# Performance work log

Measured on AMD Instinct MI355X. Metric: run time of the kernel, lower is better.

Reference implementation:

```python
import jax, jax.numpy as jnp
import numpy as np

N_NODES = 100000
N_EDGES = 1600000
IN_DIM = 64
OUT_DIM = 64
K_HEADS = 4
HEAD_DIM = OUT_DIM // K_HEADS


def setup_inputs() -> dict:
    key = jax.random.key(0)
    ks = jax.random.split(key, 12)
    x = jax.random.normal(ks[0], (N_NODES, IN_DIM), dtype=jnp.float32)
    edge_index = jax.random.randint(ks[1], (2, N_EDGES), 0, N_NODES, dtype=jnp.int64)
    edge_sign = jax.random.randint(ks[2], (N_EDGES,), 0, 2, dtype=jnp.int64)
    s = 1.0 / np.sqrt(IN_DIM)
    Wl_w = jax.random.uniform(ks[3], (OUT_DIM, IN_DIM), minval=-s, maxval=s, dtype=jnp.float32)
    Wl_b = jax.random.uniform(ks[4], (OUT_DIM,), minval=-s, maxval=s, dtype=jnp.float32)
    sign_tab = jax.random.normal(ks[5], (2, HEAD_DIM), dtype=jnp.float32)
    so = 1.0 / np.sqrt(OUT_DIM)
    Wh_w = jax.random.uniform(ks[6], (OUT_DIM, OUT_DIM), minval=-so, maxval=so, dtype=jnp.float32)
    Wh_b = jax.random.uniform(ks[7], (OUT_DIM,), minval=-so, maxval=so, dtype=jnp.float32)
    mlp_w1 = jax.random.uniform(ks[8], (OUT_DIM, OUT_DIM), minval=-so, maxval=so, dtype=jnp.float32)
    mlp_b1 = jax.random.uniform(ks[9], (OUT_DIM,), minval=-so, maxval=so, dtype=jnp.float32)
    mlp_w2 = jax.random.uniform(ks[10], (OUT_DIM, OUT_DIM), minval=-so, maxval=so, dtype=jnp.float32)
    mlp_b2 = jax.random.uniform(ks[11], (OUT_DIM,), minval=-so, maxval=so, dtype=jnp.float32)
    eps = jnp.zeros((1,), dtype=jnp.float32)
    return {"x": x, "edge_index": edge_index, "edge_sign": edge_sign,
            "Wl_w": Wl_w, "Wl_b": Wl_b, "sign_tab": sign_tab,
            "Wh_w": Wh_w, "Wh_b": Wh_b, "mlp_w1": mlp_w1, "mlp_b1": mlp_b1,
            "mlp_w2": mlp_w2, "mlp_b2": mlp_b2, "eps": eps}


def reference(x, edge_index, edge_sign, Wl_w, Wl_b, sign_tab, Wh_w, Wh_b,
              mlp_w1, mlp_b1, mlp_w2, mlp_b2, eps):
    N = x.shape[0]
    row, col = edge_index[0], edge_index[1]
    h = x @ Wl_w.T + Wl_b                              # [N, out_dim]
    hr = h.reshape(N, K_HEADS, HEAD_DIM)               # [N, K, hd]
    h_i = hr[row]                                      # [E, K, hd]
    h_j = hr[col]                                      # [E, K, hd]
    s_emb = sign_tab[edge_sign][:, None, :]            # [E, 1, hd]
    score = jnp.sum(h_i * h_j * s_emb, axis=-1)        # [E, K]
    # segment softmax over edges grouped by target node (row)
    mx = jax.ops.segment_max(score, row, num_segments=N)
    mx = jnp.where(jnp.isfinite(mx), mx, 0.0)          # empty segments -> 0
    ex = jnp.exp(score - mx[row])                      # [E, K]
    den = jax.ops.segment_sum(ex, row, num_segments=N)
    alpha = ex / (den[row] + 1e-16)                    # [E, K]
    # scatter-add weighted messages per head (vectorized over heads)
    msg = h_j * alpha[:, :, None]                      # [E, K, hd]
    aggr = jax.ops.segment_sum(msg, row, num_segments=N)  # [N, K, hd]
    m_l = aggr.reshape(N, OUT_DIM) @ Wh_w.T + Wh_b
    z = (1.0 + eps) * h + m_l
    hid = jax.nn.relu(z @ mlp_w1.T + mlp_b1)
    return hid @ mlp_w2.T + mlp_b2
```

## Files before the change

### kernel.cpp

```cpp
#include <hip/hip_runtime.h>

#define DIM 64
#define NBUCK 256
#define BSHIFT 9
#define BCAP 12288
#define CHUNK 4096

typedef __attribute__((ext_vector_type(4))) float f32x4;
typedef __attribute__((ext_vector_type(2))) float f32x2v;
typedef __attribute__((ext_vector_type(8))) short short8;

#define MFMA16(a, b, c) __builtin_amdgcn_mfma_f32_16x16x32_bf16(a, b, c, 0, 0, 0)

template <int CTRL>
__device__ __forceinline__ float qperm(float v) {
    return __int_as_float(__builtin_amdgcn_update_dpp(
        0, __float_as_int(v), CTRL, 0xF, 0xF, true));
}

__device__ __forceinline__ void cvt8(const float* f, short8& hi, short8& lo) {
#pragma unroll
    for (int e = 0; e < 8; ++e) {
        const unsigned u = __float_as_uint(f[e]);
        hi[e] = (short)(u >> 16);
        const float hf = __uint_as_float(u & 0xFFFF0000u);
        lo[e] = (short)(__float_as_uint(f[e] - hf) >> 16);
    }
}

__device__ __forceinline__ unsigned short bf16rne(float f) {
    const unsigned u = __float_as_uint(f);
    return (unsigned short)((u + 0x7FFFu + ((u >> 16) & 1u)) >> 16);
}

__global__ __launch_bounds__(256) void prep_kernel(
    const float* __restrict__ Wl, const float* __restrict__ Wh,
    const float* __restrict__ W1, const float* __restrict__ W2,
    short8* __restrict__ wf, int* __restrict__ bcursor,
    int* __restrict__ edata, int* __restrict__ offsets, int N, int E)
{
    const int tid = threadIdx.x;
    bcursor[tid] = 0;
    edata[E + tid] = 0;
    edata[E + 256 + tid] = 0;
    if (tid == 0) offsets[N] = E;
    const int m = tid >> 6, l = tid & 63;
    const float* W = (m == 0) ? Wl : (m == 1) ? Wh : (m == 2) ? W1 : W2;
    const int o = l & 15;
    const int kg = (l >> 4) * 8;
#pragma unroll
    for (int t = 0; t < 4; ++t)
#pragma unroll
        for (int s = 0; s < 2; ++s) {
            float f[8];
#pragma unroll
            for (int e = 0; e < 8; ++e)
                f[e] = W[(o + 16 * t) * DIM + 32 * s + kg + e];
            short8 hi, lo;
            cvt8(f, hi, lo);
            const int base = (((m * 4 + t) * 2 + s) * 2);
            wf[(base + 0) * 64 + l] = hi;
            wf[(base + 1) * 64 + l] = lo;
        }
}

__global__ __launch_bounds__(256, 3) void gemmbin_kernel(
    const float* __restrict__ x, const short8* __restrict__ wf,
    const float* __restrict__ bias, float* __restrict__ h,
    unsigned short* __restrict__ hb, int N,
    const int* __restrict__ ei, const int* __restrict__ sgn,
    int* __restrict__ bcursor, int* __restrict__ records, int E, int NB)
{
    if (blockIdx.x & 1) {
        const int l = threadIdx.x & 63;
        const int gw = (blockIdx.x >> 1) * 4 + (threadIdx.x >> 6);
        const int nw = NB * 4;
        const int nstrips = (N + 15) >> 4;
        const int lr = l & 15, lk = (l >> 4) * 8, lrow4 = (l >> 4) * 4;

        short8 wh_[4][2], wl_[4][2];
#pragma unroll
        for (int t = 0; t < 4; ++t)
#pragma unroll
            for (int s = 0; s < 2; ++s) {
                wh_[t][s] = wf[(((0 * 4 + t) * 2 + s) * 2 + 0) * 64 + l];
                wl_[t][s] = wf[(((0 * 4 + t) * 2 + s) * 2 + 1) * 64 + l];
            }
        float b4[4];
#pragma unroll
        for (int t = 0; t < 4; ++t) b4[t] = bias[lr + 16 * t];

        for (int strip = gw; strip < nstrips; strip += nw) {
            const int rbase = strip * 16;
            const int arow = min(rbase + lr, N - 1);
            short8 ah[2], al[2];
#pragma unroll
            for (int s = 0; s < 2; ++s) {
                const float4 p0 = *reinterpret_cast<const float4*>(x + (size_t)arow * DIM + 32 * s + lk);
                const float4 p1 = *reinterpret_cast<const float4*>(x + (size_t)arow * DIM + 32 * s + lk + 4);
                float f[8] = {p0.x, p0.y, p0.z, p0.w, p1.x, p1.y, p1.z, p1.w};
                cvt8(f, ah[s], al[s]);
            }
            f32x4 acc[4];
#pragma unroll
            for (int t = 0; t < 4; ++t) acc[t] = (f32x4){b4[t], b4[t], b4[t], b4[t]};
#pragma unroll
            for (int s = 0; s < 2; ++s) {
#pragma unroll
                for (int t = 0; t < 4; ++t) acc[t] = MFMA16(ah[s], wh_[t][s], acc[t]);
#pragma unroll
                for (int t = 0; t < 4; ++t) acc[t] = MFMA16(ah[s], wl_[t][s], acc[t]);
#pragma unroll
                for (int t = 0; t < 4; ++t) acc[t] = MFMA16(al[s], wh_[t][s], acc[t]);
            }
#pragma unroll
            for (int t = 0; t < 4; ++t)
#pragma unroll
                for (int rg = 0; rg < 4; ++rg) {
                    const int row = rbase + lrow4 + rg;
                    if (row < N) {
                        h[(size_t)row * DIM + lr + 16 * t] = acc[t][rg];
                        hb[(size_t)row * DIM + lr + 16 * t] = bf16rne(acc[t][rg]);
                    }
                }
        }
    } else {
        const int tid = threadIdx.x;
        const int base = (blockIdx.x >> 1) * CHUNK;
        __shared__ int lcnt[NBUCK];
        __shared__ int lbase[NBUCK];
        lcnt[tid] = 0;
        __syncthreads();
        const int lim = min(CHUNK, E - base);
        if (lim == CHUNK && (E & 3) == 0) {
            int r[16];
#pragma unroll
            for (int j = 0; j < 4; ++j) {
                const int4 a = *(reinterpret_cast<const int4*>(ei + base) + tid * 4 + j);
                r[4*j+0]=a.x; r[4*j+1]=a.y; r[4*j+2]=a.z; r[4*j+3]=a.w;
            }
#pragma unroll
            for (int i = 0; i < 16; ++i) atomicAdd(&lcnt[r[i] >> BSHIFT], 1);
            __syncthreads();
            const int c = lcnt[tid];
            lbase[tid] = c ? atomicAdd(&bcursor[tid], c) : 0;
            lcnt[tid] = 0;
            __syncthreads();
            int cc[16], ss[16];
#pragma unroll
            for (int j = 0; j < 4; ++j) {
                const int4 a = *(reinterpret_cast<const int4*>(ei + E + base) + tid * 4 + j);
                cc[4*j+0]=a.x; cc[4*j+1]=a.y; cc[4*j+2]=a.z; cc[4*j+3]=a.w;
                const int4 s2 = *(reinterpret_cast<const int4*>(sgn + base) + tid * 4 + j);
                ss[4*j+0]=s2.x; ss[4*j+1]=s2.y; ss[4*j+2]=s2.z; ss[4*j+3]=s2.w;
            }
#pragma unroll
            for (int half = 0; half < 2; ++half) {
                int idx[8];
#pragma unroll
                for (int i = 0; i < 8; ++i) {
                    const int e8 = half * 8 + i;
                    const int bkt = r[e8] >> BSHIFT;
                    idx[i] = lbase[bkt] + atomicAdd(&lcnt[bkt], 1);
                }
#pragma unroll
                for (int i = 0; i < 8; ++i) {
                    const int e8 = half * 8 + i;
                    const int bkt = r[e8] >> BSHIFT;
                    records[bkt * BCAP + min(idx[i], BCAP - 1)] =
                        cc[e8] | (ss[e8] << 17) | ((r[e8] & 511) << 18);
                }
            }
        } else {
            for (int k = tid; k < lim; k += 256)
                atomicAdd(&lcnt[ei[base + k] >> BSHIFT], 1);
            __syncthreads();
            const int c = lcnt[tid];
            lbase[tid] = c ? atomicAdd(&bcursor[tid], c) : 0;
            lcnt[tid] = 0;
            __syncthreads();
            for (int k = tid; k < lim; k += 256) {
                const int e = base + k;
                const int rr = ei[e];
                const int cc2 = ei[E + e];
                const int s = sgn[e];
                const int b = rr >> BSHIFT;
                const int idx = min(lbase[b] + atomicAdd(&lcnt[b], 1), BCAP - 1);
                records[b * BCAP + idx] = cc2 | (s << 17) | ((rr & 511) << 18);
            }
        }
    }
}

__device__ __forceinline__ int wave_incl_scan(int v, int lane) {
#pragma unroll
    for (int off = 1; off < 64; off <<= 1) {
        int t = __shfl_up(v, (unsigned)off, 64);
        if (lane >= off) v += t;
    }
    return v;
}

__global__ __launch_bounds__(256) void build_kernel(
    const int* __restrict__ records, const int* __restrict__ bcursor,
    int* __restrict__ offsets, int* __restrict__ edata, int N)
{
    const int b = blockIdx.x;
    const int tid = threadIdx.x, lane = tid & 63, w = tid >> 6;
    const int nbase = b << BSHIFT;
    const int nn = min(512, N - nbase);
    if (nn <= 0) return;

    __shared__ int ncnt[512];
    __shared__ int wtot[8];
    __shared__ int csrb_l[NBUCK];
    __shared__ int stag[BCAP];

    {
        const int bv = min(bcursor[tid], BCAP);
        const int inc = wave_incl_scan(bv, lane);
        if (lane == 63) wtot[w] = inc;
        __syncthreads();
        int add = 0;
#pragma unroll
        for (int i = 0; i < 4; ++i)
            if (i < w) add += wtot[i];
        csrb_l[tid] = add + inc - bv;
        __syncthreads();
    }
    const int base_csr = csrb_l[b];
    const int cnt = min(bcursor[b], BCAP);
    const int* rec = records + b * BCAP;

    ncnt[tid] = 0; ncnt[256 + tid] = 0;
    __syncthreads();
    for (int i = tid; i < cnt; i += 256)
        atomicAdd(&ncnt[rec[i] >> 18], 1);
    __syncthreads();
    const int v0 = ncnt[tid], v1 = ncnt[256 + tid];
    const int i0 = wave_incl_scan(v0, lane);
    if (lane == 63) wtot[w] = i0;
    const int i1 = wave_incl_scan(v1, lane);
    if (lane == 63) wtot[4 + w] = i1;
    __syncthreads();
    int a0 = 0, a1 = 0;
#pragma unroll
    for (int i = 0; i < 4; ++i) {
        if (i < w) { a0 += wtot[i]; a1 += wtot[4 + i]; }
    }
    const int half = wtot[0] + wtot[1] + wtot[2] + wtot[3];
    const int e0 = a0 + i0 - v0;
    const int e1 = half + a1 + i1 - v1;
    if (tid < nn)       offsets[nbase + tid]       = base_csr + e0;
    if (256 + tid < nn) offsets[nbase + 256 + tid] = base_csr + e1;
    __syncthreads();
    ncnt[tid] = e0; ncnt[256 + tid] = e1;
    __syncthreads();
    for (int i = tid; i < cnt; i += 256) {
        const int rcd = rec[i];
        const int p = atomicAdd(&ncnt[rcd >> 18], 1);
        stag[p] = (rcd & 0x1FFFF) | (((rcd >> 17) & 1) << 20);
    }
    __syncthreads();
    for (int i = tid; i < cnt; i += 256)
        edata[base_csr + i] = stag[i];
}

__global__ __launch_bounds__(256) void attntail_kernel(
    const float* __restrict__ h, const unsigned short* __restrict__ hb,
    const int* __restrict__ offsets, const int* __restrict__ edata,
    const float* __restrict__ sign_tab, const short8* __restrict__ wf,
    const float* __restrict__ bh, const float* __restrict__ b1,
    const float* __restrict__ b2, const float* __restrict__ eps,
    float* __restrict__ out, int N)
{
    __shared__ float bufA[16 * 68];
    __shared__ float bufB[16 * 68];

    const int lane = threadIdx.x & 63;
    const int w    = threadIdx.x >> 6;
    const int gl   = lane & 15;
    const int g    = lane >> 4;
    const int rbase = blockIdx.x * 16;
    const int node  = rbase + (w << 2) + g;
    const bool alive = node < N;
    const int nidx = alive ? node : 0;

    const int beg = offsets[nidx];
    const int deg = offsets[nidx + 1] - beg;

    const float4 hi = *reinterpret_cast<const float4*>(h + ((unsigned)nidx << 6) + (gl << 2));
    const float4 s0 = *reinterpret_cast<const float4*>(sign_tab + ((gl & 3) << 2));
    const float4 s1 = *reinterpret_cast<const float4*>(sign_tab + 16 + ((gl & 3) << 2));
    const f32x2v hs0a = {hi.x * s0.x, hi.y * s0.y};
    const f32x2v hs0b = {hi.z * s0.z, hi.w * s0.w};
    const f32x2v hs1a = {hi.x * s1.x, hi.y * s1.y};
    const f32x2v hs1b = {hi.z * s1.z, hi.w * s1.w};

    int maxdeg = max(deg, __shfl_xor(deg, 16, 64));
    maxdeg = max(maxdeg, __shfl_xor(maxdeg, 32, 64));

    float den = 0.f;
    f32x2v ma = {0.f, 0.f}, mb = {0.f, 0.f};
    const unsigned glb = (unsigned)(gl << 3);

    for (int e = 0; e < maxdeg; e += 8) {
        int pk[8];
#pragma unroll
        for (int u = 0; u < 8; ++u)
            pk[u] = edata[(unsigned)(beg + e + u)];
        uint2 v[8];
#pragma unroll
        for (int u = 0; u < 8; ++u) {
            unsigned off = (((unsigned)pk[u] & 0x1FFFFu) << 7) + glb;
            off = (e + u < deg) ? off : glb;
            v[u] = *reinterpret_cast<const uint2*>(
                reinterpret_cast<const char*>(hb) + off);
        }
#pragma unroll
        for (int u = 0; u < 8; ++u) {
            const f32x2v ha = {__uint_as_float(v[u].x << 16),
                               __uint_as_float(v[u].x & 0xFFFF0000u)};
            const f32x2v hc = {__uint_as_float(v[u].y << 16),
                               __uint_as_float(v[u].y & 0xFFFF0000u)};
            const bool sg = (pk[u] >> 20) & 1;
            const f32x2v wa = sg ? hs1a : hs0a;
            const f32x2v wb = sg ? hs1b : hs0b;
            const f32x2v p = wa * ha + wb * hc;
            float sc = p.x + p.y;
            sc += qperm<0xB1>(sc);
            sc += qperm<0x4E>(sc);
            const float ex = (e + u < deg) ? __expf(sc) : 0.f;
            den += ex;
            ma += ex * ha;
            mb += ex * hc;
        }
    }
    {
        const float inv = 1.0f / (den + 1e-16f);
        float* rowp = bufA + ((w << 2) + g) * 68 + (gl << 2);
        rowp[0] = ma.x * inv; rowp[1] = ma.y * inv;
        rowp[2] = mb.x * inv; rowp[3] = mb.y * inv;
    }
    __syncthreads();

    const int lr = lane & 15, lk = (lane >> 4) * 8, lrow4 = (lane >> 4) * 4;
    short8 f1h[2], f1l[2], f2h[2], f2l[2], f3h[2], f3l[2];
#pragma unroll
    for (int s = 0; s < 2; ++s) {
        f1h[s] = wf[(((1 * 4 + w) * 2 + s) * 2 + 0) * 64 + lane];
        f1l[s] = wf[(((1 * 4 + w) * 2 + s) * 2 + 1) * 64 + lane];
        f2h[s] = wf[(((2 * 4 + w) * 2 + s) * 2 + 0) * 64 + lane];
        f2l[s] = wf[(((2 * 4 + w) * 2 + s) * 2 + 1) * 64 + lane];
        f3h[s] = wf[(((3 * 4 + w) * 2 + s) * 2 + 0) * 64 + lane];
        f3l[s] = wf[(((3 * 4 + w) * 2 + s) * 2 + 1) * 64 + lane];
    }
    const float bhv = bh[lr + 16 * w];
    const float b1v = b1[lr + 16 * w];
    const float b2v = b2[lr + 16 * w];
    const float escale = 1.0f + eps[0];

    float vh[4];
#pragma unroll
    for (int rg = 0; rg < 4; ++rg)
        vh[rg] = h[(size_t)min(rbase + lrow4 + rg, N - 1) * DIM + lr + 16 * w];

    short8 ah[2], al[2];
#pragma unroll
    for (int s = 0; s < 2; ++s) {
        float f[8];
#pragma unroll
        for (int e = 0; e < 8; ++e) f[e] = bufA[lr * 68 + 32 * s + lk + e];
        cvt8(f, ah[s], al[s]);
    }
    f32x4 acc = (f32x4){bhv, bhv, bhv, bhv};
#pragma unroll
    for (int s = 0; s < 2; ++s) {
        acc = MFMA16(ah[s], f1h[s], acc);
        acc = MFMA16(ah[s], f1l[s], acc);
        acc = MFMA16(al[s], f1h[s], acc);
    }
#pragma unroll
    for (int rg = 0; rg < 4; ++rg)
        bufB[(lrow4 + rg) * 68 + lr + 16 * w] = fmaf(escale, vh[rg], acc[rg]);
    __syncthreads();

#pragma unroll
    for (int s = 0; s < 2; ++s) {
        float f[8];
#pragma unroll
        for (int e = 0; e < 8; ++e) f[e] = bufB[lr * 68 + 32 * s + lk + e];
        cvt8(f, ah[s], al[s]);
    }
    acc = (f32x4){b1v, b1v, b1v, b1v};
#pragma unroll
    for (int s = 0; s < 2; ++s) {
        acc = MFMA16(ah[s], f2h[s], acc);
        acc = MFMA16(ah[s], f2l[s], acc);
        acc = MFMA16(al[s], f2h[s], acc);
    }
#pragma unroll
    for (int rg = 0; rg < 4; ++rg)
        bufA[(lrow4 + rg) * 68 + lr + 16 * w] = fmaxf(acc[rg], 0.f);
    __syncthreads();

#pragma unroll
    for (int s = 0; s < 2; ++s) {
        float f[8];
#pragma unroll
        for (int e = 0; e < 8; ++e) f[e] = bufA[lr * 68 + 32 * s + lk + e];
        cvt8(f, ah[s], al[s]);
    }
    acc = (f32x4){b2v, b2v, b2v, b2v};
#pragma unroll
    for (int s = 0; s < 2; ++s) {
        acc = MFMA16(ah[s], f3h[s], acc);
        acc = MFMA16(ah[s], f3l[s], acc);
        acc = MFMA16(al[s], f3h[s], acc);
    }
#pragma unroll
    for (int rg = 0; rg < 4; ++rg) {
        const int row = rbase + lrow4 + rg;
        if (row < N) out[(size_t)row * DIM + lr + 16 * w] = acc[rg];
    }
}

extern "C" void kernel_launch(void* const* d_in, const int* in_sizes, int n_in,
                              void* d_out, int out_size, void* d_ws, size_t ws_size,
                              hipStream_t stream) {
    const float* x        = (const float*)d_in[0];
    const int*   ei       = (const int*)d_in[1];
    const int*   esign    = (const int*)d_in[2];
    const float* Wl_w     = (const float*)d_in[3];
    const float* Wl_b     = (const float*)d_in[4];
    const float* sign_tab = (const float*)d_in[5];
    const float* Wh_w     = (const float*)d_in[6];
    const float* Wh_b     = (const float*)d_in[7];
    const float* w1       = (const float*)d_in[8];
    const float* b1       = (const float*)d_in[9];
    const float* w2       = (const float*)d_in[10];
    const float* b2       = (const float*)d_in[11];
    const float* eps      = (const float*)d_in[12];
    float* out = (float*)d_out;

    const int N = in_sizes[0] / DIM;
    const int E = in_sizes[2];
    const int NB = (E + CHUNK - 1) / CHUNK;

    float* h            = (float*)d_ws;
    unsigned short* hb  = (unsigned short*)(h + (size_t)N * DIM);
    int*   records      = (int*)(hb + (size_t)N * DIM);
    int*   edata        = records + NBUCK * BCAP;
    int*   bcursor      = edata + (E + 520);
    int*   offsets      = bcursor + NBUCK;
    short8* wf          = (short8*)(offsets + ((N + 1 + 3) & ~3));

    prep_kernel<<<1, 256, 0, stream>>>(Wl_w, Wh_w, w1, w2, wf, bcursor,
                                       edata, offsets, N, E);

    gemmbin_kernel<<<2 * NB, 256, 0, stream>>>(x, wf, Wl_b, h, hb, N,
                                               ei, esign, bcursor, records, E, NB);

    build_kernel<<<NBUCK, 256, 0, stream>>>(records, bcursor, offsets, edata, N);

    attntail_kernel<<<(N + 15) / 16, 256, 0, stream>>>(
        h, hb, offsets, edata, sign_tab, wf, Wh_b, b1, b2, eps, out, N);
}
```

Measured before the change: 110.5 us.

## Sort edge records per chunk locally and gather bucket runs in build

```diff
diff --git a/kernel.cpp b/kernel.cpp
--- a/kernel.cpp
+++ b/kernel.cpp
@@ -64,12 +64,22 @@
         }
 }
 
+__device__ __forceinline__ int wave_incl_scan(int v, int lane) {
+#pragma unroll
+    for (int off = 1; off < 64; off <<= 1) {
+        int t = __shfl_up(v, (unsigned)off, 64);
+        if (lane >= off) v += t;
+    }
+    return v;
+}
+
 __global__ __launch_bounds__(256, 3) void gemmbin_kernel(
     const float* __restrict__ x, const short8* __restrict__ wf,
     const float* __restrict__ bias, float* __restrict__ h,
     unsigned short* __restrict__ hb, int N,
     const int* __restrict__ ei, const int* __restrict__ sgn,
-    int* __restrict__ bcursor, int* __restrict__ records, int E, int NB)
+    int* __restrict__ bcursor, int* __restrict__ records,
+    unsigned int* __restrict__ cnts, int E, int NB)
 {
     if (blockIdx.x & 1) {
         const int l = threadIdx.x & 63;
@@ -126,9 +136,13 @@
         }
     } else {
         const int tid = threadIdx.x;
-        const int base = (blockIdx.x >> 1) * CHUNK;
+        const int lane = tid & 63, w = tid >> 6;
+        const int blk = blockIdx.x >> 1;
+        const int base = blk * CHUNK;
         __shared__ int lcnt[NBUCK];
-        __shared__ int lbase[NBUCK];
+        __shared__ int lpre[NBUCK];
+        __shared__ int wtot_s[4];
+        __shared__ int stag[CHUNK];
         lcnt[tid] = 0;
         __syncthreads();
         const int lim = min(CHUNK, E - base);
@@ -142,8 +156,21 @@
 #pragma unroll
             for (int i = 0; i < 16; ++i) atomicAdd(&lcnt[r[i] >> BSHIFT], 1);
             __syncthreads();
-            const int c = lcnt[tid];
-            lbase[tid] = c ? atomicAdd(&bcursor[tid], c) : 0;
+            {
+                const int v = lcnt[tid];
+                const int inc = wave_incl_scan(v, lane);
+                if (lane == 63) wtot_s[w] = inc;
+                __syncthreads();
+                int add = 0;
+#pragma unroll
+                for (int i = 0; i < 4; ++i)
+                    if (i < w) add += wtot_s[i];
+                const int pre = add + inc - v;
+                lpre[tid] = pre;
+                cnts[blk * NBUCK + tid] = (unsigned)pre | ((unsigned)v << 16);
+                if (v) atomicAdd(&bcursor[tid], v);
+            }
+            __syncthreads();
             lcnt[tid] = 0;
             __syncthreads();
             int cc[16], ss[16];
@@ -155,28 +182,34 @@
                 ss[4*j+0]=s2.x; ss[4*j+1]=s2.y; ss[4*j+2]=s2.z; ss[4*j+3]=s2.w;
             }
 #pragma unroll
-            for (int half = 0; half < 2; ++half) {
-                int idx[8];
-#pragma unroll
-                for (int i = 0; i < 8; ++i) {
-                    const int e8 = half * 8 + i;
-                    const int bkt = r[e8] >> BSHIFT;
-                    idx[i] = lbase[bkt] + atomicAdd(&lcnt[bkt], 1);
-                }
-#pragma unroll
-                for (int i = 0; i < 8; ++i) {
-                    const int e8 = half * 8 + i;
-                    const int bkt = r[e8] >> BSHIFT;
-                    records[bkt * BCAP + min(idx[i], BCAP - 1)] =
-                        cc[e8] | (ss[e8] << 17) | ((r[e8] & 511) << 18);
-                }
-            }
+            for (int i = 0; i < 16; ++i) {
+                const int bkt = r[i] >> BSHIFT;
+                const int idx = lpre[bkt] + atomicAdd(&lcnt[bkt], 1);
+                stag[idx] = cc[i] | (ss[i] << 17) | ((r[i] & 511) << 18);
+            }
+            __syncthreads();
+            for (int i = tid * 4; i < CHUNK; i += 1024)
+                *reinterpret_cast<int4*>(records + base + i) =
+                    *reinterpret_cast<const int4*>(stag + i);
         } else {
             for (int k = tid; k < lim; k += 256)
                 atomicAdd(&lcnt[ei[base + k] >> BSHIFT], 1);
             __syncthreads();
-            const int c = lcnt[tid];
-            lbase[tid] = c ? atomicAdd(&bcursor[tid], c) : 0;
+            {
+                const int v = lcnt[tid];
+                const int inc = wave_incl_scan(v, lane);
+                if (lane == 63) wtot_s[w] = inc;
+                __syncthreads();
+                int add = 0;
+#pragma unroll
+                for (int i = 0; i < 4; ++i)
+                    if (i < w) add += wtot_s[i];
+                const int pre = add + inc - v;
+                lpre[tid] = pre;
+                cnts[blk * NBUCK + tid] = (unsigned)pre | ((unsigned)v << 16);
+                if (v) atomicAdd(&bcursor[tid], v);
+            }
+            __syncthreads();
             lcnt[tid] = 0;
             __syncthreads();
             for (int k = tid; k < lim; k += 256) {
@@ -185,25 +218,20 @@
                 const int cc2 = ei[E + e];
                 const int s = sgn[e];
                 const int b = rr >> BSHIFT;
-                const int idx = min(lbase[b] + atomicAdd(&lcnt[b], 1), BCAP - 1);
-                records[b * BCAP + idx] = cc2 | (s << 17) | ((rr & 511) << 18);
-            }
+                const int idx = lpre[b] + atomicAdd(&lcnt[b], 1);
+                stag[idx] = cc2 | (s << 17) | ((rr & 511) << 18);
+            }
+            __syncthreads();
+            for (int i = tid; i < lim; i += 256)
+                records[base + i] = stag[i];
         }
     }
 }
 
-__device__ __forceinline__ int wave_incl_scan(int v, int lane) {
-#pragma unroll
-    for (int off = 1; off < 64; off <<= 1) {
-        int t = __shfl_up(v, (unsigned)off, 64);
-        if (lane >= off) v += t;
-    }
-    return v;
-}
-
 __global__ __launch_bounds__(256) void build_kernel(
-    const int* __restrict__ records, const int* __restrict__ bcursor,
-    int* __restrict__ offsets, int* __restrict__ edata, int N)
+    const int* __restrict__ records, const unsigned int* __restrict__ cnts,
+    const int* __restrict__ bcursor,
+    int* __restrict__ offsets, int* __restrict__ edata, int N, int NB)
 {
     const int b = blockIdx.x;
     const int tid = threadIdx.x, lane = tid & 63, w = tid >> 6;
@@ -211,10 +239,11 @@
     const int nn = min(512, N - nbase);
     if (nn <= 0) return;
 
+    __shared__ int stag[BCAP];
     __shared__ int ncnt[512];
     __shared__ int wtot[8];
     __shared__ int csrb_l[NBUCK];
-    __shared__ int stag[BCAP];
+    __shared__ int blkoff[512];
 
     {
         const int bv = min(bcursor[tid], BCAP);
@@ -229,13 +258,45 @@
         __syncthreads();
     }
     const int base_csr = csrb_l[b];
-    const int cnt = min(bcursor[b], BCAP);
-    const int* rec = records + b * BCAP;
+    const int cntb = min(bcursor[b], BCAP);
+
+    const unsigned pc0 = (tid < NB) ? cnts[tid * NBUCK + b] : 0u;
+    const unsigned pc1 = (256 + tid < NB) ? cnts[(256 + tid) * NBUCK + b] : 0u;
+    const int c0 = (int)(pc0 >> 16), c1 = (int)(pc1 >> 16);
+    __syncthreads();
+    {
+        const int i0 = wave_incl_scan(c0, lane);
+        if (lane == 63) wtot[w] = i0;
+        const int i1 = wave_incl_scan(c1, lane);
+        if (lane == 63) wtot[4 + w] = i1;
+        __syncthreads();
+        int a0 = 0, a1 = 0;
+#pragma unroll
+        for (int i = 0; i < 4; ++i) {
+            if (i < w) { a0 += wtot[i]; a1 += wtot[4 + i]; }
+        }
+        const int half = wtot[0] + wtot[1] + wtot[2] + wtot[3];
+        blkoff[tid] = a0 + i0 - c0;
+        blkoff[256 + tid] = half + a1 + i1 - c1;
+    }
+    __syncthreads();
+
+    if (tid < NB) {
+        const int* src = records + tid * CHUNK + (int)(pc0 & 0xFFFFu);
+        const int dst = blkoff[tid];
+        for (int i = 0; i < c0; ++i) stag[dst + i] = src[i];
+    }
+    if (256 + tid < NB) {
+        const int* src = records + (256 + tid) * CHUNK + (int)(pc1 & 0xFFFFu);
+        const int dst = blkoff[256 + tid];
+        for (int i = 0; i < c1; ++i) stag[dst + i] = src[i];
+    }
+    __syncthreads();
 
     ncnt[tid] = 0; ncnt[256 + tid] = 0;
     __syncthreads();
-    for (int i = tid; i < cnt; i += 256)
-        atomicAdd(&ncnt[rec[i] >> 18], 1);
+    for (int i = tid; i < cntb; i += 256)
+        atomicAdd(&ncnt[stag[i] >> 18], 1);
     __syncthreads();
     const int v0 = ncnt[tid], v1 = ncnt[256 + tid];
     const int i0 = wave_incl_scan(v0, lane);
@@ -256,14 +317,11 @@
     __syncthreads();
     ncnt[tid] = e0; ncnt[256 + tid] = e1;
     __syncthreads();
-    for (int i = tid; i < cnt; i += 256) {
-        const int rcd = rec[i];
+    for (int i = tid; i < cntb; i += 256) {
+        const int rcd = stag[i];
         const int p = atomicAdd(&ncnt[rcd >> 18], 1);
-        stag[p] = (rcd & 0x1FFFF) | (((rcd >> 17) & 1) << 20);
-    }
-    __syncthreads();
-    for (int i = tid; i < cnt; i += 256)
-        edata[base_csr + i] = stag[i];
+        edata[base_csr + p] = (rcd & 0x1FFFF) | (((rcd >> 17) & 1) << 20);
+    }
 }
 
 __global__ __launch_bounds__(256) void attntail_kernel(
@@ -290,12 +348,14 @@
     const int deg = offsets[nidx + 1] - beg;
 
     const float4 hi = *reinterpret_cast<const float4*>(h + ((unsigned)nidx << 6) + (gl << 2));
+    const float L2E = 1.44269504f;
+    const float4 hiL = make_float4(hi.x * L2E, hi.y * L2E, hi.z * L2E, hi.w * L2E);
     const float4 s0 = *reinterpret_cast<const float4*>(sign_tab + ((gl & 3) << 2));
     const float4 s1 = *reinterpret_cast<const float4*>(sign_tab + 16 + ((gl & 3) << 2));
-    const f32x2v hs0a = {hi.x * s0.x, hi.y * s0.y};
-    const f32x2v hs0b = {hi.z * s0.z, hi.w * s0.w};
-    const f32x2v hs1a = {hi.x * s1.x, hi.y * s1.y};
-    const f32x2v hs1b = {hi.z * s1.z, hi.w * s1.w};
+    const f32x2v hs0a = {hiL.x * s0.x, hiL.y * s0.y};
+    const f32x2v hs0b = {hiL.z * s0.z, hiL.w * s0.w};
+    const f32x2v hs1a = {hiL.x * s1.x, hiL.y * s1.y};
+    const f32x2v hs1b = {hiL.z * s1.z, hiL.w * s1.w};
 
     int maxdeg = max(deg, __shfl_xor(deg, 16, 64));
     maxdeg = max(maxdeg, __shfl_xor(maxdeg, 32, 64));
@@ -330,7 +390,7 @@
             float sc = p.x + p.y;
             sc += qperm<0xB1>(sc);
             sc += qperm<0x4E>(sc);
-            const float ex = (e + u < deg) ? __expf(sc) : 0.f;
+            const float ex = (e + u < deg) ? exp2f(sc) : 0.f;
             den += ex;
             ma += ex * ha;
             mb += ex * hc;
@@ -450,18 +510,21 @@
     float* h            = (float*)d_ws;
     unsigned short* hb  = (unsigned short*)(h + (size_t)N * DIM);
     int*   records      = (int*)(hb + (size_t)N * DIM);
-    int*   edata        = records + NBUCK * BCAP;
+    int*   edata        = records + (size_t)NB * CHUNK;
     int*   bcursor      = edata + (E + 520);
     int*   offsets      = bcursor + NBUCK;
     short8* wf          = (short8*)(offsets + ((N + 1 + 3) & ~3));
+    unsigned int* cnts  = (unsigned int*)(wf + 4096);
 
     prep_kernel<<<1, 256, 0, stream>>>(Wl_w, Wh_w, w1, w2, wf, bcursor,
                                        edata, offsets, N, E);
 
     gemmbin_kernel<<<2 * NB, 256, 0, stream>>>(x, wf, Wl_b, h, hb, N,
-                                               ei, esign, bcursor, records, E, NB);
-
-    build_kernel<<<NBUCK, 256, 0, stream>>>(records, bcursor, offsets, edata, N);
+                                               ei, esign, bcursor, records,
+                                               cnts, E, NB);
+
+    build_kernel<<<NBUCK, 256, 0, stream>>>(records, cnts, bcursor,
+                                            offsets, edata, N, NB);
 
     attntail_kernel<<<(N + 15) / 16, 256, 0, stream>>>(
         h, hb, offsets, edata, sign_tab, wf, Wh_b, b1, b2, eps, out, N);
```

Result: no change. 109.6 us (-0.8%).
